# Kernel optimization log

Hardware: AMD Instinct MI355X
Metric: run time of the kernel (lower is better)

Reference implementation:

```python
import jax, jax.numpy as jnp
import numpy as np

B, N, M, T, D, NH = 64, 1024, 32, 8, 512, 8
OUT = 1000
NSO, NSA = N // 4, N // 8
DH = D // NH


def _conv(x, w, b):
    y = jax.lax.conv_general_dilated(x, w, (1, 1), 'SAME', dimension_numbers=('NCHW', 'OIHW', 'NCHW'))
    return y + b[None, :, None, None]


def _bn(x, g, b):
    # BatchNorm2d in train mode: per-batch statistics over (B, H, W)
    m = x.mean(axis=(0, 2, 3), keepdims=True)
    v = x.var(axis=(0, 2, 3), keepdims=True)
    return (x - m) * jax.lax.rsqrt(v + 1e-5) * g[None, :, None, None] + b[None, :, None, None]


def _mp2(x):
    b_, c, h, w = x.shape
    return x.reshape(b_, c, h // 2, 2, w // 2, 2).max(axis=(3, 5))


def _ln(x, g, b):
    m = x.mean(-1, keepdims=True)
    v = x.var(-1, keepdims=True)
    return (x - m) * jax.lax.rsqrt(v + 1e-5) * g + b


def _glu(x):
    a, b = jnp.split(x, 2, axis=-1)
    return a * jax.nn.sigmoid(b)


def setup_inputs():
    ks = iter(jax.random.split(jax.random.key(0), 64))

    def nrm(shape, fan_in):
        return jax.random.normal(next(ks), shape, jnp.float32) / np.float32(np.sqrt(fan_in))

    inp = {}
    inp['x'] = jax.random.normal(next(ks), (B, 3, 64, 64), jnp.float32)
    inp['c1w'] = nrm((16, 3, 3, 3), 27); inp['c1b'] = jnp.zeros((16,))
    inp['bn1g'] = jnp.ones((16,)); inp['bn1b'] = jnp.zeros((16,))
    inp['c2w'] = nrm((32, 16, 3, 3), 144); inp['c2b'] = jnp.zeros((32,))
    inp['bn2g'] = jnp.ones((32,)); inp['bn2b'] = jnp.zeros((32,))
    inp['c3w'] = nrm((64, 32, 3, 3), 288); inp['c3b'] = jnp.zeros((64,))
    inp['bn3g'] = jnp.ones((64,)); inp['bn3b'] = jnp.zeros((64,))
    inp['c4w'] = nrm((64, 64, 3, 3), 576); inp['c4b'] = jnp.zeros((64,))
    inp['bn4g'] = jnp.ones((64,)); inp['bn4b'] = jnp.zeros((64,))
    inp['fc1w'] = nrm((256, 256), 256); inp['fc1b'] = jnp.zeros((256,))
    inp['fc2w'] = nrm((128, D), 128); inp['fc2b'] = jnp.zeros((D,))
    inp['kvw'] = nrm((D, D), D); inp['kvb'] = jnp.zeros((D,))
    inp['kvlg'] = jnp.ones((D,)); inp['kvlb'] = jnp.zeros((D,))
    inp['synw'] = nrm((D + N, 2 * N), D + N); inp['synb'] = jnp.zeros((2 * N,))
    inp['synlg'] = jnp.ones((N,)); inp['synlb'] = jnp.zeros((N,))
    inp['nlm_w1'] = nrm((N, M, 256), M); inp['nlm_b1'] = jnp.zeros((N, 256))
    inp['nlm_w2'] = nrm((N, 128), 128); inp['nlm_b2'] = jnp.zeros((N,))
    inp['start_act'] = nrm((N,), N)
    inp['start_trace'] = nrm((N, M), N + M)
    inp['dec_a'] = jax.random.uniform(next(ks), (NSA,), jnp.float32, 0.0, 3.0)
    inp['dec_o'] = jax.random.uniform(next(ks), (NSO,), jnp.float32, 0.0, 3.0)
    inp['qw'] = nrm((NSA, D), NSA); inp['qb'] = jnp.zeros((D,))
    inp['attn_inw'] = nrm((D, 3 * D), D); inp['attn_inb'] = jnp.zeros((3 * D,))
    inp['attn_ow'] = nrm((D, D), D); inp['attn_ob'] = jnp.zeros((D,))
    inp['op_w1'] = nrm((NSO, 256), NSO); inp['op_b1'] = jnp.zeros((256,))
    inp['op_l1g'] = jnp.ones((256,)); inp['op_l1b'] = jnp.zeros((256,))
    inp['op_w2'] = nrm((256, 64), 256); inp['op_b2'] = jnp.zeros((64,))
    inp['op_l2g'] = jnp.ones((64,)); inp['op_l2b'] = jnp.zeros((64,))
    inp['op_w3'] = nrm((64, OUT), 64); inp['op_b3'] = jnp.zeros((OUT,))
    inp['aL'] = jax.random.randint(next(ks), (NSA,), 0, N)
    inp['aR'] = jax.random.randint(next(ks), (NSA,), 0, N)
    inp['oL'] = jax.random.randint(next(ks), (NSO,), 0, N)
    inp['oR'] = jax.random.randint(next(ks), (NSO,), 0, N)
    inp['task_idx'] = 0
    return inp


def _forward(x, c1w, c1b, bn1g, bn1b, c2w, c2b, bn2g, bn2b, c3w, c3b, bn3g, bn3b, c4w, c4b, bn4g, bn4b, fc1w, fc1b, fc2w, fc2b, kvw, kvb, kvlg, kvlb, synw, synb, synlg, synlb, nlm_w1, nlm_b1, nlm_w2, nlm_b2, start_act, start_trace, dec_a, dec_o, qw, qb, attn_inw, attn_inb, attn_ow, attn_ob, op_w1, op_b1, op_l1g, op_l1b, op_w2, op_b2, op_l2g, op_l2b, op_w3, op_b3, aL, aR, oL, oR):
    # --- AdaptiveCNNEncoder (3-channel branch) ---
    h = jax.nn.relu(_bn(_conv(x, c1w, c1b), bn1g, bn1b))
    h = jax.nn.relu(_bn(_conv(h, c2w, c2b), bn2g, bn2b))
    h = _mp2(h)
    h = jax.nn.relu(_bn(_conv(h, c3w, c3b), bn3g, bn3b))
    h = _mp2(h)
    h = jax.nn.relu(_bn(_conv(h, c4w, c4b), bn4g, bn4b))
    b_, c, hh, ww = h.shape
    # AdaptiveAvgPool2d((2,2)): mean over equal blocks (16x16 -> 2x2)
    h = h.reshape(b_, c, 2, hh // 2, 2, ww // 2).mean(axis=(3, 5)).reshape(b_, c * 4)
    enc = _glu(h @ fc1w + fc1b) @ fc2w + fc2b            # (B, D)
    kv = _ln(enc @ kvw + kvb, kvlg, kvlb)                # single kv token

    Wq, Wk, Wv = jnp.split(attn_inw, 3, axis=1)
    bq, bk, bv = jnp.split(attn_inb, 3)
    kh = (kv @ Wk + bk).reshape(B, NH, DH)
    vh = (kv @ Wv + bv).reshape(B, NH, DH)

    r_a = jnp.exp(-jnp.clip(dec_a, 0.0, 15.0))           # (NSA,)
    r_o = jnp.exp(-jnp.clip(dec_o, 0.0, 15.0))           # (NSO,)

    act0 = jnp.broadcast_to(start_act, (B, N))
    trace0 = jnp.broadcast_to(start_trace, (B, N, M))
    ao0 = act0[:, oL] * act0[:, oR]                      # initial out-sync accumulators
    bo0 = jnp.ones_like(ao0)
    inv_log_out = np.float32(1.0 / np.log(OUT))
    inv_sqrt_dh = np.float32(1.0 / np.sqrt(DH))

    def tick(carry, t):
        act, trace, aa, ba, ao, bo = carry
        pp = act[:, aL] * act[:, aR]
        first = (t == 0)
        aa = jnp.where(first, pp, r_a * aa + pp)
        ba = jnp.where(first, jnp.ones_like(ba), r_a * ba + 1.0)
        sync_a = aa * jax.lax.rsqrt(ba + 1e-8)
        qv = sync_a @ qw + qb
        qh = (qv @ Wq + bq).reshape(B, NH, DH)
        logits = jnp.einsum('bhd,bhd->bh', qh, kh) * inv_sqrt_dh
        w = jax.nn.softmax(logits[..., None], axis=-1)[..., 0]  # single key -> ones
        attn_out = (w[..., None] * vh).reshape(B, D) @ attn_ow + attn_ob
        pre = jnp.concatenate([attn_out, act], axis=-1)
        state = _ln(_glu(pre @ synw + synb), synlg, synlb)
        trace = jnp.concatenate([trace[:, :, 1:], state[:, :, None]], axis=-1)
        # per-neuron private MLPs, batched: (B,N,M)x(N,M,256) -> GLU -> (N,128) -> scalar
        hid = _glu(jnp.einsum('bnm,nmh->bnh', trace, nlm_w1) + nlm_b1)
        act = jnp.einsum('bnh,nh->bn', hid, nlm_w2) + nlm_b2
        po = act[:, oL] * act[:, oR]
        ao = r_o * ao + po
        bo = r_o * bo + 1.0
        sync_o = ao * jax.lax.rsqrt(bo + 1e-8)
        h1 = jax.nn.relu(_ln(sync_o @ op_w1 + op_b1, op_l1g, op_l1b))
        h2 = jax.nn.relu(_ln(h1 @ op_w2 + op_b2, op_l2g, op_l2b))
        pred = h2 @ op_w3 + op_b3
        p = jax.nn.softmax(pred, axis=-1)
        ent = -jnp.sum(p * jnp.log(p + 1e-10), axis=-1)
        ne = ent * inv_log_out
        cert = jnp.stack([ne, 1.0 - ne], axis=-1)
        return (act, trace, aa, ba, ao, bo), (pred, cert)

    carry0 = (act0, trace0, jnp.zeros((B, NSA), jnp.float32), jnp.zeros((B, NSA), jnp.float32), ao0, bo0)
    _, (preds, certs) = jax.lax.scan(tick, carry0, jnp.arange(T))
    return jnp.transpose(preds, (1, 2, 0)), jnp.transpose(certs, (1, 2, 0))


def reference(x, c1w, c1b, bn1g, bn1b, c2w, c2b, bn2g, bn2b, c3w, c3b, bn3g, bn3b, c4w, c4b, bn4g, bn4b, fc1w, fc1b, fc2w, fc2b, kvw, kvb, kvlg, kvlb, synw, synb, synlg, synlb, nlm_w1, nlm_b1, nlm_w2, nlm_b2, start_act, start_trace, dec_a, dec_o, qw, qb, attn_inw, attn_inb, attn_ow, attn_ob, op_w1, op_b1, op_l1g, op_l1b, op_w2, op_b2, op_l2g, op_l2b, op_w3, op_b3, aL, aR, oL, oR, task_idx):
    del task_idx  # single task; all task-indexed params are for task 0
    return _forward(x, c1w, c1b, bn1g, bn1b, c2w, c2b, bn2g, bn2b, c3w, c3b, bn3g, bn3b, c4w, c4b, bn4g, bn4b, fc1w, fc1b, fc2w, fc2b, kvw, kvb, kvlg, kvlb, synw, synb, synlg, synlb, nlm_w1, nlm_b1, nlm_w2, nlm_b2, start_act, start_trace, dec_a, dec_o, qw, qb, attn_inw, attn_inb, attn_ow, attn_ob, op_w1, op_b1, op_l1g, op_l1b, op_w2, op_b2, op_l2g, op_l2b, op_w3, op_b3, aL, aR, oL, oR)
```

## Files before the change

kernel.cpp:

```cpp
#include <hip/hip_runtime.h>
#include <math.h>

constexpr int B_ = 64, N_ = 1024, M_ = 32, T_ = 8;
constexpr int OUT_ = 1000, NSO_ = 256;

#define DEVFN __device__ __forceinline__

typedef __attribute__((ext_vector_type(8))) short bf16x8;
typedef __attribute__((ext_vector_type(4))) float f32x4;

DEVFN float blockReduceSum(float v, float* buf) {
  int t = threadIdx.x;
  buf[t] = v; __syncthreads();
  for (int off = blockDim.x >> 1; off > 0; off >>= 1) {
    if (t < off) buf[t] += buf[t + off];
    __syncthreads();
  }
  float r = buf[0];
  __syncthreads();
  return r;
}

DEVFN float sigmoidf_(float x) { return 1.f / (1.f + __expf(-x)); }

DEVFN unsigned short f2bf(float f) {
  unsigned u = __float_as_uint(f);
  unsigned r = (u + 0x7FFFu + ((u >> 16) & 1u)) >> 16;
  return (unsigned short)r;
}
DEVFN float bf2f(unsigned short h) { return __uint_as_float((unsigned)h << 16); }

template<int NW>
DEVFN float bsum(float v, float* red) {
  #pragma unroll
  for (int o = 32; o > 0; o >>= 1) v += __shfl_xor(v, o);
  int w = threadIdx.x >> 6, ln = threadIdx.x & 63;
  if (ln == 0) red[w] = v;
  __syncthreads();
  if (w == 0) {
    float x = (ln < NW) ? red[ln] : 0.f;
    #pragma unroll
    for (int o = 8; o > 0; o >>= 1) x += __shfl_xor(x, o);
    if (ln == 0) red[0] = x;
  }
  __syncthreads();
  float r = red[0];
  __syncthreads();
  return r;
}

template<int NW>
DEVFN float bmax(float v, float* red) {
  #pragma unroll
  for (int o = 32; o > 0; o >>= 1) v = fmaxf(v, __shfl_xor(v, o));
  int w = threadIdx.x >> 6, ln = threadIdx.x & 63;
  if (ln == 0) red[w] = v;
  __syncthreads();
  if (w == 0) {
    float x = (ln < NW) ? red[ln] : -INFINITY;
    #pragma unroll
    for (int o = 8; o > 0; o >>= 1) x = fmaxf(x, __shfl_xor(x, o));
    if (ln == 0) red[0] = x;
  }
  __syncthreads();
  float r = red[0];
  __syncthreads();
  return r;
}

DEVFN void bn_ssl(float2* ssl, const float* bnpart, const float* g, const float* bb,
                  int C, int ns, float inv_n) {
  for (int c = threadIdx.x; c < C; c += blockDim.x) {
    float s1 = 0.f, s2 = 0.f;
    for (int s = 0; s < ns; ++s) { s1 += bnpart[(c * ns + s) * 2]; s2 += bnpart[(c * ns + s) * 2 + 1]; }
    float m = s1 * inv_n;
    float var = s2 * inv_n - m * m;
    float rstd = rsqrtf(var + 1e-5f);
    float sc = g[c] * rstd;
    ssl[c] = make_float2(sc, bb[c] - m * sc);
  }
}

__global__ __launch_bounds__(256)
void k_wprep(const float* __restrict__ c2w, const float* __restrict__ c3w,
             const float* __restrict__ c4w, unsigned short* __restrict__ wt2,
             unsigned short* __restrict__ wt3, unsigned short* __restrict__ wt4) {
  int i = blockIdx.x * 256 + threadIdx.x;
  if (i < 5120) {
    int tap = i / 512, co = (i / 16) % 32, ci = i & 15;
    wt2[i] = (tap < 9) ? f2bf(c2w[(co * 16 + ci) * 9 + tap]) : 0;
  } else if (i < 5120 + 18432) {
    int j = i - 5120;
    int tap = j / 2048, co = (j / 32) % 64, ci = j & 31;
    wt3[j] = f2bf(c3w[(co * 32 + ci) * 9 + tap]);
  } else if (i < 5120 + 18432 + 36864) {
    int j = i - 5120 - 18432;
    int tap = j / 4096, co = (j / 64) % 64, ci = j & 63;
    wt4[j] = f2bf(c4w[(co * 64 + ci) * 9 + tap]);
  }
}

__global__ __launch_bounds__(256)
void k_w1t(const float* __restrict__ w1, unsigned short* __restrict__ w1t) {
  int n = blockIdx.x;
  __shared__ float tile[32][260];
  const float* src = w1 + (size_t)n * 8192;
  for (int i = threadIdx.x; i < 8192; i += 256)
    tile[i >> 8][i & 255] = src[i];
  __syncthreads();
  int c = threadIdx.x;
  unsigned short* dst = w1t + ((size_t)n * 256 + c) * 32;
  #pragma unroll
  for (int q = 0; q < 8; ++q) {
    ushort4 o;
    o.x = f2bf(tile[q * 4 + 0][c]); o.y = f2bf(tile[q * 4 + 1][c]);
    o.z = f2bf(tile[q * 4 + 2][c]); o.w = f2bf(tile[q * 4 + 3][c]);
    *reinterpret_cast<ushort4*>(dst + q * 4) = o;
  }
}

__global__ __launch_bounds__(256)
void k_synwt(const float* __restrict__ synw2, unsigned short* __restrict__ Bt) {
  int j0 = blockIdx.x * 64, k0 = blockIdx.y * 64;
  __shared__ float tile[64][65];
  for (int i = threadIdx.x; i < 4096; i += 256) {
    int kk = i >> 6, jj = i & 63;
    tile[kk][jj] = synw2[(size_t)(k0 + kk) * 2048 + j0 + jj];
  }
  __syncthreads();
  int jj = threadIdx.x >> 2, kq = (threadIdx.x & 3) * 16;
  unsigned short* dst = Bt + (size_t)(j0 + jj) * 1024 + k0 + kq;
  #pragma unroll
  for (int q = 0; q < 4; ++q) {
    ushort4 o;
    o.x = f2bf(tile[kq + q * 4 + 0][jj]); o.y = f2bf(tile[kq + q * 4 + 1][jj]);
    o.z = f2bf(tile[kq + q * 4 + 2][jj]); o.w = f2bf(tile[kq + q * 4 + 3][jj]);
    *reinterpret_cast<ushort4*>(dst + q * 4) = o;
  }
}

__global__ __launch_bounds__(256)
void k_conv1(const float* __restrict__ in, const float* __restrict__ wgl,
             unsigned short* __restrict__ outp) {
  constexpr int HW = 64, TY = 4, XV = 4, XQ = 16, CPT = 4;
  __shared__ __align__(16) float ins[3][TY + 2][HW + 8];
  const int b = blockIdx.x, y0 = blockIdx.y * TY, tid = threadIdx.x;
  const int sp = tid & 63;
  const int cg = __builtin_amdgcn_readfirstlane(tid >> 6);
  const int xq = sp % XQ, yr = sp / XQ, x0 = xq * XV;
  float acc[CPT][XV];
  #pragma unroll
  for (int j = 0; j < CPT; ++j)
    #pragma unroll
    for (int k = 0; k < XV; ++k) acc[j][k] = 0.f;
  constexpr int NEL = 3 * (TY + 2) * (HW + 8);
  for (int i = tid; i < NEL; i += 256) {
    int col = i % (HW + 8), row = (i / (HW + 8)) % (TY + 2), ci = i / ((HW + 8) * (TY + 2));
    int gx = col - 4, gy = y0 + row - 1;
    float v = 0.f;
    if (gx >= 0 && gx < HW && gy >= 0 && gy < HW)
      v = in[((size_t)(b * 3 + ci) * HW + gy) * HW + gx];
    ins[ci][row][col] = v;
  }
  __syncthreads();
  for (int ci = 0; ci < 3; ++ci) {
    const float* wci = wgl + ((size_t)(cg * CPT) * 3 + ci) * 9;
    #pragma unroll
    for (int dy = 0; dy < 3; ++dy) {
      const float* r = &ins[ci][yr + dy][x0 + 4];
      float win[6];
      win[0] = r[-1];
      float4 m = *reinterpret_cast<const float4*>(r);
      win[1] = m.x; win[2] = m.y; win[3] = m.z; win[4] = m.w;
      win[5] = r[4];
      #pragma unroll
      for (int j = 0; j < CPT; ++j) {
        const float* wj = wci + (size_t)j * 27 + dy * 3;
        float w0 = wj[0], w1 = wj[1], w2 = wj[2];
        #pragma unroll
        for (int k = 0; k < XV; ++k)
          acc[j][k] = fmaf(win[k], w0, fmaf(win[k + 1], w1, fmaf(win[k + 2], w2, acc[j][k])));
      }
    }
  }
  #pragma unroll
  for (int j = 0; j < CPT; ++j) {
    unsigned short* op = outp + (((size_t)b * 16 + cg * CPT + j) * HW + y0 + yr) * HW + x0;
    ushort4 o;
    o.x = f2bf(acc[j][0]); o.y = f2bf(acc[j][1]); o.z = f2bf(acc[j][2]); o.w = f2bf(acc[j][3]);
    *reinterpret_cast<ushort4*>(op) = o;
  }
}

__global__ __launch_bounds__(256)
void k_conv2_mfma(const unsigned short* __restrict__ in, const unsigned short* __restrict__ wt2,
                  const float* __restrict__ bnpart, const float* __restrict__ bng,
                  const float* __restrict__ bnb, unsigned short* __restrict__ outp) {
  const int b = blockIdx.x, y = blockIdx.y;
  const int tid = threadIdx.x;
  const int w = tid >> 6, lane = tid & 63;
  const int col = lane & 15, kg = lane >> 4;
  const int p0 = w * 16;
  __shared__ unsigned short lds[3][68][16];
  __shared__ float2 ssl[16];
  bn_ssl(ssl, bnpart, bng, bnb, 16, 32, 1.f / (float)(B_ * 4096));
  __syncthreads();
  for (int i = tid; i < 3 * 66 * 16; i += 256) {
    int px = i % 66, row = (i / 66) % 3, ci = i / 198;
    int gy = y + row - 1, gx = px - 1;
    float v = 0.f;
    if (gy >= 0 && gy < 64 && gx >= 0 && gx < 64) {
      float2 s = ssl[ci];
      v = fmaxf(fmaf(bf2f(in[((size_t)(b * 16 + ci) * 64 + gy) * 64 + gx]), s.x, s.y), 0.f);
    }
    lds[row][px][ci] = f2bf(v);
  }
  __syncthreads();
  f32x4 acc0 = {0.f, 0.f, 0.f, 0.f}, acc1 = {0.f, 0.f, 0.f, 0.f};
  const int tsel = kg >> 1, ci0 = (kg & 1) * 8;
  #pragma unroll
  for (int p = 0; p < 5; ++p) {
    int tap = 2 * p + tsel;
    int dy = (tap < 9) ? tap / 3 : 0;
    int dx = (tap < 9) ? tap % 3 : 0;
    bf16x8 af = *reinterpret_cast<const bf16x8*>(&lds[dy][p0 + col + dx][ci0]);
    bf16x8 b0 = *reinterpret_cast<const bf16x8*>(wt2 + ((size_t)tap * 32 + col) * 16 + ci0);
    bf16x8 b1 = *reinterpret_cast<const bf16x8*>(wt2 + ((size_t)tap * 32 + 16 + col) * 16 + ci0);
    acc0 = __builtin_amdgcn_mfma_f32_16x16x32_bf16(af, b0, acc0, 0, 0, 0);
    acc1 = __builtin_amdgcn_mfma_f32_16x16x32_bf16(af, b1, acc1, 0, 0, 0);
  }
  int px = p0 + kg * 4;
  ushort4 o0, o1;
  o0.x = f2bf(acc0[0]); o0.y = f2bf(acc0[1]); o0.z = f2bf(acc0[2]); o0.w = f2bf(acc0[3]);
  o1.x = f2bf(acc1[0]); o1.y = f2bf(acc1[1]); o1.z = f2bf(acc1[2]); o1.w = f2bf(acc1[3]);
  *reinterpret_cast<ushort4*>(outp + ((size_t)(b * 32 + col) * 64 + y) * 64 + px) = o0;
  *reinterpret_cast<ushort4*>(outp + ((size_t)(b * 32 + 16 + col) * 64 + y) * 64 + px) = o1;
}

__global__ __launch_bounds__(256)
void k_conv3_mfma(const unsigned short* __restrict__ in, const unsigned short* __restrict__ wt3,
                  const float* __restrict__ bnpart, const float* __restrict__ bng,
                  const float* __restrict__ bnb, unsigned short* __restrict__ outp) {
  const int b = blockIdx.x, y0 = blockIdx.y * 2;
  const int tid = threadIdx.x;
  const int w = tid >> 6, lane = tid & 63;
  const int col = lane & 15, kg = lane >> 4;
  const int yloc = w >> 1, p0 = (w & 1) * 16;
  __shared__ unsigned short lds[4][34][40];
  __shared__ float2 ssl[32];
  bn_ssl(ssl, bnpart, bng, bnb, 32, 32, 1.f / (float)(B_ * 4096));
  __syncthreads();
  for (int i = tid; i < 4 * 34 * 32; i += 256) {
    int px = i % 34, row = (i / 34) % 4, ci = i / 136;
    int gy = y0 + row - 1, gx = px - 1;
    float v = 0.f;
    if (gy >= 0 && gy < 32 && gx >= 0 && gx < 32) {
      float2 s = ssl[ci];
      size_t base = ((size_t)(b * 32 + ci) * 64 + 2 * gy) * 64 + 2 * gx;
      float r0 = fmaf(bf2f(in[base]),      s.x, s.y);
      float r1 = fmaf(bf2f(in[base + 1]),  s.x, s.y);
      float r2 = fmaf(bf2f(in[base + 64]), s.x, s.y);
      float r3 = fmaf(bf2f(in[base + 65]), s.x, s.y);
      v = fmaxf(fmaxf(fmaxf(r0, r1), fmaxf(r2, r3)), 0.f);
    }
    lds[row][px][ci] = f2bf(v);
  }
  __syncthreads();
  f32x4 acc[4];
  #pragma unroll
  for (int c = 0; c < 4; ++c) acc[c] = (f32x4){0.f, 0.f, 0.f, 0.f};
  #pragma unroll
  for (int tap = 0; tap < 9; ++tap) {
    int dy = tap / 3, dx = tap % 3;
    bf16x8 af = *reinterpret_cast<const bf16x8*>(&lds[yloc + dy][p0 + col + dx][kg * 8]);
    #pragma unroll
    for (int c = 0; c < 4; ++c) {
      bf16x8 bfr = *reinterpret_cast<const bf16x8*>(wt3 + ((size_t)tap * 64 + c * 16 + col) * 32 + kg * 8);
      acc[c] = __builtin_amdgcn_mfma_f32_16x16x32_bf16(af, bfr, acc[c], 0, 0, 0);
    }
  }
  int yy = y0 + yloc, px = p0 + kg * 4;
  #pragma unroll
  for (int c = 0; c < 4; ++c) {
    ushort4 o;
    o.x = f2bf(acc[c][0]); o.y = f2bf(acc[c][1]); o.z = f2bf(acc[c][2]); o.w = f2bf(acc[c][3]);
    *reinterpret_cast<ushort4*>(outp + ((size_t)(b * 64 + c * 16 + col) * 32 + yy) * 32 + px) = o;
  }
}

__global__ __launch_bounds__(128)
void k_conv4_mfma(const unsigned short* __restrict__ in, const unsigned short* __restrict__ wt4,
                  const float* __restrict__ bnpart, const float* __restrict__ bng,
                  const float* __restrict__ bnb, unsigned short* __restrict__ outp) {
  const int b = blockIdx.x, y0 = blockIdx.y * 2;
  const int tid = threadIdx.x;
  const int w = tid >> 6, lane = tid & 63;
  const int col = lane & 15, kg = lane >> 4;
  __shared__ unsigned short lds[4][18][72];
  __shared__ float2 ssl[64];
  bn_ssl(ssl, bnpart, bng, bnb, 64, 16, 1.f / (float)(B_ * 1024));
  __syncthreads();
  for (int i = tid; i < 4 * 18 * 64; i += 128) {
    int px = i % 18, row = (i / 18) % 4, ci = i / 72;
    int gy = y0 + row - 1, gx = px - 1;
    float v = 0.f;
    if (gy >= 0 && gy < 16 && gx >= 0 && gx < 16) {
      float2 s = ssl[ci];
      size_t base = ((size_t)(b * 64 + ci) * 32 + 2 * gy) * 32 + 2 * gx;
      float r0 = fmaf(bf2f(in[base]),      s.x, s.y);
      float r1 = fmaf(bf2f(in[base + 1]),  s.x, s.y);
      float r2 = fmaf(bf2f(in[base + 32]), s.x, s.y);
      float r3 = fmaf(bf2f(in[base + 33]), s.x, s.y);
      v = fmaxf(fmaxf(fmaxf(r0, r1), fmaxf(r2, r3)), 0.f);
    }
    lds[row][px][ci] = f2bf(v);
  }
  __syncthreads();
  f32x4 acc[4];
  #pragma unroll
  for (int c = 0; c < 4; ++c) acc[c] = (f32x4){0.f, 0.f, 0.f, 0.f};
  #pragma unroll
  for (int tap = 0; tap < 9; ++tap) {
    int dy = tap / 3, dx = tap % 3;
    #pragma unroll
    for (int kc = 0; kc < 2; ++kc) {
      bf16x8 af = *reinterpret_cast<const bf16x8*>(&lds[w + dy][col + dx][kc * 32 + kg * 8]);
      #pragma unroll
      for (int c = 0; c < 4; ++c) {
        bf16x8 bfr = *reinterpret_cast<const bf16x8*>(wt4 + ((size_t)tap * 64 + c * 16 + col) * 64 + kc * 32 + kg * 8);
        acc[c] = __builtin_amdgcn_mfma_f32_16x16x32_bf16(af, bfr, acc[c], 0, 0, 0);
      }
    }
  }
  int yy = y0 + w, px = kg * 4;
  #pragma unroll
  for (int c = 0; c < 4; ++c) {
    ushort4 o;
    o.x = f2bf(acc[c][0]); o.y = f2bf(acc[c][1]); o.z = f2bf(acc[c][2]); o.w = f2bf(acc[c][3]);
    *reinterpret_cast<ushort4*>(outp + ((size_t)(b * 64 + c * 16 + col) * 16 + yy) * 16 + px) = o;
  }
}

template<int C, int HW2>
__global__ __launch_bounds__(256)
void k_bn_stats_bf(const unsigned short* __restrict__ x, float* __restrict__ part) {
  int c = blockIdx.x, s = blockIdx.y, ns = gridDim.y;
  const int Np2 = B_ * HW2 / 2;
  float s1 = 0.f, s2 = 0.f;
  for (int ii = s * 256 + threadIdx.x; ii < Np2; ii += ns * 256) {
    int b = ii / (HW2 / 2), p2 = ii % (HW2 / 2);
    const unsigned short* pp = x + ((size_t)b * C + c) * HW2 + p2 * 2;
    unsigned u = *reinterpret_cast<const unsigned*>(pp);
    float v0 = __uint_as_float(u << 16);
    float v1 = __uint_as_float(u & 0xFFFF0000u);
    s1 += v0 + v1; s2 += v0 * v0 + v1 * v1;
  }
  __shared__ float r1[256], r2[256];
  r1[threadIdx.x] = s1; r2[threadIdx.x] = s2; __syncthreads();
  for (int off = 128; off > 0; off >>= 1) {
    if (threadIdx.x < off) { r1[threadIdx.x] += r1[threadIdx.x + off]; r2[threadIdx.x] += r2[threadIdx.x + off]; }
    __syncthreads();
  }
  if (threadIdx.x == 0) {
    part[(c * ns + s) * 2 + 0] = r1[0];
    part[(c * ns + s) * 2 + 1] = r2[0];
  }
}

__global__ __launch_bounds__(256)
void k_avgpool_bn_bf(const unsigned short* __restrict__ x, const float* __restrict__ bnpart,
                     const float* __restrict__ g, const float* __restrict__ bb,
                     float* __restrict__ outp) {
  __shared__ float2 ssl[64];
  bn_ssl(ssl, bnpart, g, bb, 64, 8, 1.f / (float)(B_ * 256));
  __syncthreads();
  int idx = blockIdx.x * 256 + threadIdx.x;
  int b = idx >> 8;
  int r = idx & 255;
  int c = r >> 2, i = (r >> 1) & 1, j = r & 1;
  float2 s = ssl[c];
  const unsigned short* p = x + ((size_t)(b * 64 + c) * 16 + i * 8) * 16 + j * 8;
  float sum = 0.f;
  #pragma unroll
  for (int yy = 0; yy < 8; ++yy)
    #pragma unroll
    for (int xx = 0; xx < 8; ++xx)
      sum += fmaxf(fmaf(bf2f(p[yy * 16 + xx]), s.x, s.y), 0.f);
  outp[idx] = sum * (1.f / 64.f);
}

template<int K, int NOUT>
__global__ __launch_bounds__(256)
void k_gemm_part(const float* __restrict__ A, const float* __restrict__ W, int ldw,
                 float* __restrict__ part) {
  int jt = blockIdx.x, ks = blockIdx.y;
  int k0 = ks * 64;
  __shared__ float As[64][65];
  for (int i = threadIdx.x; i < 4096; i += 256) {
    int r = i >> 6, c = i & 63;
    As[r][c] = A[(size_t)r * K + k0 + c];
  }
  __syncthreads();
  int jsub = threadIdx.x & 31;
  int bg = threadIdx.x >> 5;
  int j = jt * 32 + jsub;
  float acc[8] = {0.f, 0.f, 0.f, 0.f, 0.f, 0.f, 0.f, 0.f};
  const float* wp = W + (size_t)k0 * ldw + j;
  #pragma unroll 8
  for (int kk = 0; kk < 64; ++kk) {
    float w = wp[(size_t)kk * ldw];
    #pragma unroll
    for (int r = 0; r < 8; ++r) acc[r] = fmaf(As[bg * 8 + r][kk], w, acc[r]);
  }
  float* pp = part + (size_t)ks * 64 * NOUT + j;
  #pragma unroll
  for (int r = 0; r < 8; ++r) pp[(size_t)(bg * 8 + r) * NOUT] = acc[r];
}

__global__ __launch_bounds__(256)
void k_syn_mfma(const unsigned short* __restrict__ Abf, const unsigned short* __restrict__ Bt,
                float* __restrict__ part) {
  const int jt = blockIdx.x, ks = blockIdx.y;
  const int w = threadIdx.x >> 6, lane = threadIdx.x & 63;
  const int col = lane & 15, kg = lane >> 4;
  const int jcol = jt * 64 + w * 16 + col;
  const int k0 = ks * 256;
  f32x4 acc[4];
  #pragma unroll
  for (int mt = 0; mt < 4; ++mt) acc[mt] = (f32x4){0.f, 0.f, 0.f, 0.f};
  #pragma unroll
  for (int kb = 0; kb < 8; ++kb) {
    const int kk = k0 + kb * 32 + kg * 8;
    bf16x8 bfr = *reinterpret_cast<const bf16x8*>(Bt + (size_t)jcol * 1024 + kk);
    #pragma unroll
    for (int mt = 0; mt < 4; ++mt) {
      bf16x8 a = *reinterpret_cast<const bf16x8*>(Abf + (size_t)(mt * 16 + col) * 1024 + kk);
      acc[mt] = __builtin_amdgcn_mfma_f32_16x16x32_bf16(a, bfr, acc[mt], 0, 0, 0);
    }
  }
  #pragma unroll
  for (int mt = 0; mt < 4; ++mt) {
    int b0 = mt * 16 + kg * 4;
    #pragma unroll
    for (int r = 0; r < 4; ++r)
      part[((size_t)ks * 64 + b0 + r) * 2048 + jcol] = acc[mt][r];
  }
}

template<int NOUT, int NO_FIN, int KS, bool GLU_, bool LN_>
__global__ __launch_bounds__(256)
void k_fc_reduce(const float* __restrict__ part, const float* __restrict__ bias, int bstride,
                 const float* __restrict__ lng, const float* __restrict__ lnb,
                 float* __restrict__ outp) {
  constexpr int R = (NO_FIN + 255) / 256;
  int b = blockIdx.x, t = threadIdx.x;
  const float* bp = bias + (size_t)b * bstride;
  float v[R];
  #pragma unroll
  for (int r = 0; r < R; ++r) {
    int j = t + r * 256;
    if (j < NO_FIN) {
      float za = bp[j];
      float zb = GLU_ ? bp[j + NO_FIN] : 0.f;
      #pragma unroll
      for (int ks = 0; ks < KS; ++ks) {
        const float* pr = part + ((size_t)ks * 64 + b) * NOUT;
        za += pr[j];
        if (GLU_) zb += pr[j + NO_FIN];
      }
      v[r] = GLU_ ? za * sigmoidf_(zb) : za;
    } else v[r] = 0.f;
  }
  if (LN_) {
    __shared__ float red[256];
    float s1 = 0.f, s2 = 0.f;
    #pragma unroll
    for (int r = 0; r < R; ++r) { s1 += v[r]; s2 += v[r] * v[r]; }
    s1 = blockReduceSum(s1, red);
    s2 = blockReduceSum(s2, red);
    float mu = s1 / (float)NO_FIN;
    float rstd = rsqrtf(s2 / (float)NO_FIN - mu * mu + 1e-5f);
    #pragma unroll
    for (int r = 0; r < R; ++r) {
      int j = t + r * 256;
      if (j < NO_FIN) outp[(size_t)b * NO_FIN + j] = fmaf((v[r] - mu) * rstd, lng[j], lnb[j]);
    }
  } else {
    #pragma unroll
    for (int r = 0; r < R; ++r) {
      int j = t + r * 256;
      if (j < NO_FIN) outp[(size_t)b * NO_FIN + j] = v[r];
    }
  }
}

__global__ __launch_bounds__(1024)
void k_syn_reduce(const float* __restrict__ part, const float* __restrict__ syncst,
                  const float* __restrict__ g, const float* __restrict__ bb,
                  unsigned short* __restrict__ trace, int slot) {
  int b = blockIdx.x, t = threadIdx.x;
  __shared__ float red[16];
  float za = syncst[b * 2048 + t];
  float zb = syncst[b * 2048 + 1024 + t];
  #pragma unroll
  for (int ks = 0; ks < 4; ++ks) {
    const float* pr = part + ((size_t)ks * 64 + b) * 2048;
    za += pr[t];
    zb += pr[t + 1024];
  }
  float v = za * sigmoidf_(zb);
  float s1 = bsum<16>(v, red);
  float s2 = bsum<16>(v * v, red);
  float mu = s1 * (1.f / 1024.f);
  float rstd = rsqrtf(s2 * (1.f / 1024.f) - mu * mu + 1e-5f);
  trace[((size_t)t * 64 + b) * 32 + slot] = f2bf(fmaf((v - mu) * rstd, g[t], bb[t]));
}

__global__ __launch_bounds__(256)
void k_init(const float* __restrict__ sa, const float* __restrict__ st,
            const int* __restrict__ oL, const int* __restrict__ oR,
            float* __restrict__ act, unsigned short* __restrict__ act_bf,
            unsigned short* __restrict__ trace,
            float* __restrict__ ao, float* __restrict__ bo) {
  int idx = blockIdx.x * 256 + threadIdx.x;
  if (idx < B_ * N_ * M_) {
    int n = idx >> 11, m = idx & 31;
    trace[idx] = f2bf(st[n * 32 + m]);
  }
  if (idx < B_ * N_) {
    float v = sa[idx % N_];
    act[idx] = v;
    act_bf[idx] = f2bf(v);
  }
  if (idx < B_ * NSO_) {
    int i = idx % NSO_;
    ao[idx] = sa[oL[i]] * sa[oR[i]];
    bo[idx] = 1.f;
  }
}

__global__ __launch_bounds__(128)
void k_nlm_mfma(const unsigned short* __restrict__ trace, const unsigned short* __restrict__ w1t,
                const float* __restrict__ b1, const float* __restrict__ w2,
                const float* __restrict__ b2, float* __restrict__ act,
                unsigned short* __restrict__ act_bf, int tick) {
  const int w = threadIdx.x >> 6, lane = threadIdx.x & 63;
  const int n = blockIdx.x * 2 + w;
  const int col = lane & 15, kg = lane >> 4;
  __shared__ __align__(16) unsigned short ldsA[2][64][40];
  {
    const uint4* src = reinterpret_cast<const uint4*>(trace + ((size_t)n * 64 + lane) * 32);
    uint4 r0 = src[0], r1 = src[1], r2 = src[2], r3 = src[3];
    uint4* d = reinterpret_cast<uint4*>(&ldsA[w][lane][0]);
    d[0] = r0; d[1] = r1; d[2] = r2; d[3] = r3;
  }
  bf16x8 bf[16];
  float b1v[16], w2v[8];
  #pragma unroll
  for (int nt = 0; nt < 16; ++nt) {
    bf[nt] = *reinterpret_cast<const bf16x8*>(w1t + (((size_t)n * 256 + nt * 16 + col) * 32 + kg * 8));
    b1v[nt] = b1[n * 256 + nt * 16 + col];
  }
  #pragma unroll
  for (int nt = 0; nt < 8; ++nt) w2v[nt] = w2[n * 128 + nt * 16 + col];
  const float b2n = b2[n];
  const int kbase = kg * 8 + ((tick + 1) & 31);
  __syncthreads();
  #pragma unroll
  for (int mt = 0; mt < 4; ++mt) {
    const int brow = mt * 16 + col;
    bf16x8 af;
    #pragma unroll
    for (int j = 0; j < 8; ++j)
      af[j] = (short)ldsA[w][brow][(kbase + j) & 31];
    f32x4 acc[16];
    #pragma unroll
    for (int nt = 0; nt < 16; ++nt)
      acc[nt] = __builtin_amdgcn_mfma_f32_16x16x32_bf16(af, bf[nt], (f32x4){0.f, 0.f, 0.f, 0.f}, 0, 0, 0);
    float v0 = 0.f, v1 = 0.f, v2 = 0.f, v3 = 0.f;
    #pragma unroll
    for (int nt = 0; nt < 8; ++nt) {
      f32x4 za = acc[nt], zb = acc[nt + 8];
      float ba = b1v[nt], bg = b1v[nt + 8], wv = w2v[nt];
      v0 = fmaf((za[0] + ba) * sigmoidf_(zb[0] + bg), wv, v0);
      v1 = fmaf((za[1] + ba) * sigmoidf_(zb[1] + bg), wv, v1);
      v2 = fmaf((za[2] + ba) * sigmoidf_(zb[2] + bg), wv, v2);
      v3 = fmaf((za[3] + ba) * sigmoidf_(zb[3] + bg), wv, v3);
    }
    #pragma unroll
    for (int o = 1; o <= 8; o <<= 1) {
      v0 += __shfl_xor(v0, o); v1 += __shfl_xor(v1, o);
      v2 += __shfl_xor(v2, o); v3 += __shfl_xor(v3, o);
    }
    if (col == 0) {
      int b0 = mt * 16 + kg * 4;
      float r0 = v0 + b2n, r1 = v1 + b2n, r2 = v2 + b2n, r3 = v3 + b2n;
      act[(size_t)(b0 + 0) * 1024 + n] = r0;
      act[(size_t)(b0 + 1) * 1024 + n] = r1;
      act[(size_t)(b0 + 2) * 1024 + n] = r2;
      act[(size_t)(b0 + 3) * 1024 + n] = r3;
      act_bf[(size_t)(b0 + 0) * 1024 + n] = f2bf(r0);
      act_bf[(size_t)(b0 + 1) * 1024 + n] = f2bf(r1);
      act_bf[(size_t)(b0 + 2) * 1024 + n] = f2bf(r2);
      act_bf[(size_t)(b0 + 3) * 1024 + n] = f2bf(r3);
    }
  }
}

__global__ __launch_bounds__(1024)
void k_outpath(const float* __restrict__ act, float* __restrict__ ao, float* __restrict__ bo,
               const float* __restrict__ dec_o, const int* __restrict__ oL, const int* __restrict__ oR,
               const float* __restrict__ opw1, const float* __restrict__ opb1,
               const float* __restrict__ l1g, const float* __restrict__ l1b,
               const float* __restrict__ opw2, const float* __restrict__ opb2,
               const float* __restrict__ l2g, const float* __restrict__ l2b,
               const float* __restrict__ opw3, const float* __restrict__ opb3,
               float* __restrict__ outp, int tick) {
  int b = blockIdx.x, t = threadIdx.x;
  __shared__ float red[16];
  __shared__ float syo[256], h1s[256], h2s[64];
  __shared__ float zp1[4][256];
  __shared__ float zp2[16][64];
  const float* actb = act + (size_t)b * 1024;
  if (t < 256) {
    float po = actb[oL[t]] * actb[oR[t]];
    float r = __expf(-fminf(fmaxf(dec_o[t], 0.f), 15.f));
    int ai = b * 256 + t;
    float av = fmaf(r, ao[ai], po);
    float bv = fmaf(r, bo[ai], 1.f);
    ao[ai] = av; bo[ai] = bv;
    syo[t] = av * rsqrtf(bv + 1e-8f);
  }
  __syncthreads();
  {
    int j = t & 255, ks = t >> 8;
    float z = 0.f;
    const float* wcol = opw1 + j;
    #pragma unroll 8
    for (int k = ks * 64; k < ks * 64 + 64; ++k) z = fmaf(syo[k], wcol[k * 256], z);
    zp1[ks][j] = z;
  }
  __syncthreads();
  float h1v = 0.f;
  if (t < 256) h1v = zp1[0][t] + zp1[1][t] + zp1[2][t] + zp1[3][t] + opb1[t];
  float s1 = bsum<16>(t < 256 ? h1v : 0.f, red);
  float s2 = bsum<16>(t < 256 ? h1v * h1v : 0.f, red);
  if (t < 256) {
    float mu = s1 * (1.f / 256.f);
    float rstd = rsqrtf(s2 * (1.f / 256.f) - mu * mu + 1e-5f);
    h1s[t] = fmaxf(fmaf((h1v - mu) * rstd, l1g[t], l1b[t]), 0.f);
  }
  __syncthreads();
  {
    int j = t & 63, ks = t >> 6;
    float z = 0.f;
    const float* wcol = opw2 + j;
    #pragma unroll
    for (int k = ks * 16; k < ks * 16 + 16; ++k) z = fmaf(h1s[k], wcol[k * 64], z);
    zp2[ks][j] = z;
  }
  __syncthreads();
  if (t < 64) {
    float z2 = opb2[t];
    #pragma unroll
    for (int ks = 0; ks < 16; ++ks) z2 += zp2[ks][t];
    float a1 = z2, a2 = z2 * z2;
    #pragma unroll
    for (int o = 32; o > 0; o >>= 1) { a1 += __shfl_xor(a1, o); a2 += __shfl_xor(a2, o); }
    float mu2 = a1 * (1.f / 64.f);
    float rs2 = rsqrtf(a2 * (1.f / 64.f) - mu2 * mu2 + 1e-5f);
    h2s[t] = fmaxf(fmaf((z2 - mu2) * rs2, l2g[t], l2b[t]), 0.f);
  }
  __syncthreads();
  float z3 = 0.f;
  if (t < OUT_) {
    z3 = opb3[t];
    const float* wcol = opw3 + t;
    #pragma unroll 8
    for (int k = 0; k < 64; ++k) z3 = fmaf(h2s[k], wcol[k * OUT_], z3);
    outp[(size_t)b * (OUT_ * T_) + (size_t)t * T_ + tick] = z3;
  }
  float mx = bmax<16>(t < OUT_ ? z3 : -INFINITY, red);
  float e = (t < OUT_) ? __expf(z3 - mx) : 0.f;
  float S = bsum<16>(e, red);
  float inv = 1.f / S;
  float ep = 0.f;
  if (t < OUT_) {
    float p = e * inv;
    ep = p * __logf(p + 1e-10f);
  }
  float ent = -bsum<16>(ep, red);
  if (t == 0) {
    float ne = ent * (1.f / logf(1000.f));
    outp[(size_t)B_ * OUT_ * T_ + (size_t)b * 2 * T_ + tick]      = ne;
    outp[(size_t)B_ * OUT_ * T_ + (size_t)b * 2 * T_ + T_ + tick] = 1.f - ne;
  }
}

extern "C" void kernel_launch(void* const* d_in, const int* in_sizes, int n_in,
                              void* d_out, int out_size, void* d_ws, size_t ws_size,
                              hipStream_t stream) {
  (void)in_sizes; (void)n_in; (void)out_size; (void)ws_size;
  const float* x      = (const float*)d_in[0];
  const float* c1w    = (const float*)d_in[1];
  const float* bn1g   = (const float*)d_in[3];
  const float* bn1b   = (const float*)d_in[4];
  const float* c2w    = (const float*)d_in[5];
  const float* bn2g   = (const float*)d_in[7];
  const float* bn2b   = (const float*)d_in[8];
  const float* c3w    = (const float*)d_in[9];
  const float* bn3g   = (const float*)d_in[11];
  const float* bn3b   = (const float*)d_in[12];
  const float* c4w    = (const float*)d_in[13];
  const float* bn4g   = (const float*)d_in[15];
  const float* bn4b   = (const float*)d_in[16];
  const float* fc1w   = (const float*)d_in[17];
  const float* fc1b   = (const float*)d_in[18];
  const float* fc2w   = (const float*)d_in[19];
  const float* fc2b   = (const float*)d_in[20];
  const float* kvw    = (const float*)d_in[21];
  const float* kvb    = (const float*)d_in[22];
  const float* kvlg   = (const float*)d_in[23];
  const float* kvlb   = (const float*)d_in[24];
  const float* synw   = (const float*)d_in[25];
  const float* synb   = (const float*)d_in[26];
  const float* synlg  = (const float*)d_in[27];
  const float* synlb  = (const float*)d_in[28];
  const float* nlmw1  = (const float*)d_in[29];
  const float* nlmb1  = (const float*)d_in[30];
  const float* nlmw2  = (const float*)d_in[31];
  const float* nlmb2  = (const float*)d_in[32];
  const float* sact   = (const float*)d_in[33];
  const float* strc   = (const float*)d_in[34];
  const float* dec_o  = (const float*)d_in[36];
  const float* attn_inw = (const float*)d_in[39];
  const float* attn_inb = (const float*)d_in[40];
  const float* attn_ow  = (const float*)d_in[41];
  const float* attn_ob  = (const float*)d_in[42];
  const float* opw1   = (const float*)d_in[43];
  const float* opb1   = (const float*)d_in[44];
  const float* opl1g  = (const float*)d_in[45];
  const float* opl1b  = (const float*)d_in[46];
  const float* opw2   = (const float*)d_in[47];
  const float* opb2   = (const float*)d_in[48];
  const float* opl2g  = (const float*)d_in[49];
  const float* opl2b  = (const float*)d_in[50];
  const float* opw3   = (const float*)d_in[51];
  const float* opb3   = (const float*)d_in[52];
  const int*   oL     = (const int*)d_in[55];
  const int*   oR     = (const int*)d_in[56];
  float* outp = (float*)d_out;
  float* ws   = (float*)d_ws;

  unsigned short* c1raw_bf = (unsigned short*)(ws + 8388608);
  unsigned short* c2raw_bf = (unsigned short*)ws;
  unsigned short* c3raw_bf = (unsigned short*)(ws + 8388608);
  unsigned short* c4raw_bf = (unsigned short*)ws;
  float* part  = ws + 4194304;
  unsigned short* trace_bf = (unsigned short*)(ws + 6291456);
  float* act   = ws + 8388608;
  float* syncst= ws + 8454144;
  float* pooled= ws + 8585216;
  float* ench  = ws + 8601600;
  float* enc   = ws + 8609792;
  float* kvbuf = ws + 8642560;
  float* vhbuf = ws + 8675328;
  float* aout  = ws + 8708096;
  float* ao    = ws + 8740864;
  float* bo    = ws + 8757248;
  unsigned short* w1t_bf   = (unsigned short*)(ws + 8777728);
  unsigned short* synw2t_bf= (unsigned short*)(ws + 12972032);
  unsigned short* wt2 = (unsigned short*)(ws + 14061568);
  unsigned short* wt3 = (unsigned short*)(ws + 14064128);
  unsigned short* wt4 = (unsigned short*)(ws + 14073344);
  float* bnpart = ws + 14091776;
  unsigned short* act_bf = (unsigned short*)(ws + 14095872);

  k_wprep<<<236,256,0,stream>>>(c2w, c3w, c4w, wt2, wt3, wt4);

  k_conv1<<<dim3(64,16),256,0,stream>>>(x, c1w, c1raw_bf);
  k_bn_stats_bf<16,4096><<<dim3(16,32),256,0,stream>>>(c1raw_bf, bnpart);

  k_conv2_mfma<<<dim3(64,64),256,0,stream>>>(c1raw_bf, wt2, bnpart, bn1g, bn1b, c2raw_bf);
  k_bn_stats_bf<32,4096><<<dim3(32,32),256,0,stream>>>(c2raw_bf, bnpart);

  k_conv3_mfma<<<dim3(64,16),256,0,stream>>>(c2raw_bf, wt3, bnpart, bn2g, bn2b, c3raw_bf);
  k_bn_stats_bf<64,1024><<<dim3(64,16),256,0,stream>>>(c3raw_bf, bnpart);

  k_conv4_mfma<<<dim3(64,8),128,0,stream>>>(c3raw_bf, wt4, bnpart, bn3g, bn3b, c4raw_bf);

  k_w1t<<<1024,256,0,stream>>>(nlmw1, w1t_bf);
  k_synwt<<<dim3(32,16),256,0,stream>>>(synw + (size_t)512 * 2048, synw2t_bf);

  k_bn_stats_bf<64,256><<<dim3(64,8),256,0,stream>>>(c4raw_bf, bnpart);
  k_avgpool_bn_bf<<<64,256,0,stream>>>(c4raw_bf, bnpart, bn4g, bn4b, pooled);

  k_gemm_part<256,256><<<dim3(8,4),256,0,stream>>>(pooled, fc1w, 256, part);
  k_fc_reduce<256,128,4,true,false><<<64,256,0,stream>>>(part, fc1b, 0, nullptr, nullptr, ench);
  k_gemm_part<128,512><<<dim3(16,2),256,0,stream>>>(ench, fc2w, 512, part);
  k_fc_reduce<512,512,2,false,false><<<64,256,0,stream>>>(part, fc2b, 0, nullptr, nullptr, enc);
  k_gemm_part<512,512><<<dim3(16,8),256,0,stream>>>(enc, kvw, 512, part);
  k_fc_reduce<512,512,8,false,true><<<64,256,0,stream>>>(part, kvb, 0, kvlg, kvlb, kvbuf);
  k_gemm_part<512,512><<<dim3(16,8),256,0,stream>>>(kvbuf, attn_inw + 1024, 1536, part);
  k_fc_reduce<512,512,8,false,false><<<64,256,0,stream>>>(part, attn_inb + 1024, 0, nullptr, nullptr, vhbuf);
  k_gemm_part<512,512><<<dim3(16,8),256,0,stream>>>(vhbuf, attn_ow, 512, part);
  k_fc_reduce<512,512,8,false,false><<<64,256,0,stream>>>(part, attn_ob, 0, nullptr, nullptr, aout);
  k_gemm_part<512,2048><<<dim3(64,8),256,0,stream>>>(aout, synw, 2048, part);
  k_fc_reduce<2048,2048,8,false,false><<<64,256,0,stream>>>(part, synb, 0, nullptr, nullptr, syncst);

  k_init<<<8192,256,0,stream>>>(sact, strc, oL, oR, act, act_bf, trace_bf, ao, bo);

  for (int t = 0; t < T_; ++t) {
    k_syn_mfma<<<dim3(32,4),256,0,stream>>>(act_bf, synw2t_bf, part);
    k_syn_reduce<<<64,1024,0,stream>>>(part, syncst, synlg, synlb, trace_bf, t);
    k_nlm_mfma<<<512,128,0,stream>>>(trace_bf, w1t_bf, nlmb1, nlmw2, nlmb2, act, act_bf, t);
    k_outpath<<<64,1024,0,stream>>>(act, ao, bo, dec_o, oL, oR,
                                    opw1, opb1, opl1g, opl1b,
                                    opw2, opb2, opl2g, opl2b,
                                    opw3, opb3, outp, t);
  }
}
```

Before: 527.0 us.

## Fuse encoder FC chain into single per-batch kernel

```diff
diff --git a/kernel.cpp b/kernel.cpp
--- a/kernel.cpp
+++ b/kernel.cpp
@@ -8,18 +8,6 @@
 
 typedef __attribute__((ext_vector_type(8))) short bf16x8;
 typedef __attribute__((ext_vector_type(4))) float f32x4;
-
-DEVFN float blockReduceSum(float v, float* buf) {
-  int t = threadIdx.x;
-  buf[t] = v; __syncthreads();
-  for (int off = blockDim.x >> 1; off > 0; off >>= 1) {
-    if (t < off) buf[t] += buf[t + off];
-    __syncthreads();
-  }
-  float r = buf[0];
-  __syncthreads();
-  return r;
-}
 
 DEVFN float sigmoidf_(float x) { return 1.f / (1.f + __expf(-x)); }
 
@@ -389,32 +377,99 @@
   outp[idx] = sum * (1.f / 64.f);
 }
 
-template<int K, int NOUT>
-__global__ __launch_bounds__(256)
-void k_gemm_part(const float* __restrict__ A, const float* __restrict__ W, int ldw,
-                 float* __restrict__ part) {
-  int jt = blockIdx.x, ks = blockIdx.y;
-  int k0 = ks * 64;
-  __shared__ float As[64][65];
-  for (int i = threadIdx.x; i < 4096; i += 256) {
-    int r = i >> 6, c = i & 63;
-    As[r][c] = A[(size_t)r * K + k0 + c];
-  }
-  __syncthreads();
-  int jsub = threadIdx.x & 31;
-  int bg = threadIdx.x >> 5;
-  int j = jt * 32 + jsub;
-  float acc[8] = {0.f, 0.f, 0.f, 0.f, 0.f, 0.f, 0.f, 0.f};
-  const float* wp = W + (size_t)k0 * ldw + j;
-  #pragma unroll 8
-  for (int kk = 0; kk < 64; ++kk) {
-    float w = wp[(size_t)kk * ldw];
-    #pragma unroll
-    for (int r = 0; r < 8; ++r) acc[r] = fmaf(As[bg * 8 + r][kk], w, acc[r]);
-  }
-  float* pp = part + (size_t)ks * 64 * NOUT + j;
-  #pragma unroll
-  for (int r = 0; r < 8; ++r) pp[(size_t)(bg * 8 + r) * NOUT] = acc[r];
+__global__ __launch_bounds__(1024)
+void k_encfc(const float* __restrict__ pooled,
+             const float* __restrict__ fc1w, const float* __restrict__ fc1b,
+             const float* __restrict__ fc2w, const float* __restrict__ fc2b,
+             const float* __restrict__ kvw, const float* __restrict__ kvb,
+             const float* __restrict__ kvlg, const float* __restrict__ kvlb,
+             const float* __restrict__ attn_inw, const float* __restrict__ attn_inb,
+             const float* __restrict__ attn_ow, const float* __restrict__ attn_ob,
+             const float* __restrict__ synw, const float* __restrict__ synb,
+             float* __restrict__ syncst) {
+  const int b = blockIdx.x, t = threadIdx.x;
+  __shared__ float a[256], ench[128], enc[512], kv[512], vh[512], ao_[512];
+  __shared__ float zp[1024];
+  __shared__ float red[16];
+  if (t < 256) a[t] = pooled[b * 256 + t];
+  __syncthreads();
+  {
+    int j = t & 255, ks = t >> 8;
+    float z = 0.f;
+    const float* w = fc1w + j;
+    #pragma unroll 8
+    for (int k = ks * 64; k < ks * 64 + 64; ++k) z = fmaf(a[k], w[k * 256], z);
+    zp[ks * 256 + j] = z;
+  }
+  __syncthreads();
+  if (t < 128) {
+    float za = zp[t] + zp[256 + t] + zp[512 + t] + zp[768 + t] + fc1b[t];
+    int j2 = t + 128;
+    float zb = zp[j2] + zp[256 + j2] + zp[512 + j2] + zp[768 + j2] + fc1b[j2];
+    ench[t] = za * sigmoidf_(zb);
+  }
+  __syncthreads();
+  {
+    int j = t & 511, ks = t >> 9;
+    float z = 0.f;
+    const float* w = fc2w + j;
+    #pragma unroll 8
+    for (int k = ks * 64; k < ks * 64 + 64; ++k) z = fmaf(ench[k], w[k * 512], z);
+    zp[ks * 512 + j] = z;
+  }
+  __syncthreads();
+  if (t < 512) enc[t] = zp[t] + zp[512 + t] + fc2b[t];
+  __syncthreads();
+  {
+    int j = t & 511, ks = t >> 9;
+    float z = 0.f;
+    const float* w = kvw + j;
+    #pragma unroll 8
+    for (int k = ks * 256; k < ks * 256 + 256; ++k) z = fmaf(enc[k], w[k * 512], z);
+    zp[ks * 512 + j] = z;
+  }
+  __syncthreads();
+  float zkv = 0.f;
+  if (t < 512) zkv = zp[t] + zp[512 + t] + kvb[t];
+  float s1 = bsum<16>(t < 512 ? zkv : 0.f, red);
+  float s2 = bsum<16>(t < 512 ? zkv * zkv : 0.f, red);
+  if (t < 512) {
+    float mu = s1 * (1.f / 512.f);
+    float rstd = rsqrtf(s2 * (1.f / 512.f) - mu * mu + 1e-5f);
+    kv[t] = fmaf((zkv - mu) * rstd, kvlg[t], kvlb[t]);
+  }
+  __syncthreads();
+  {
+    int j = t & 511, ks = t >> 9;
+    float z = 0.f;
+    const float* w = attn_inw + 1024 + j;
+    #pragma unroll 8
+    for (int k = ks * 256; k < ks * 256 + 256; ++k) z = fmaf(kv[k], w[(size_t)k * 1536], z);
+    zp[ks * 512 + j] = z;
+  }
+  __syncthreads();
+  if (t < 512) vh[t] = zp[t] + zp[512 + t] + attn_inb[1024 + t];
+  __syncthreads();
+  {
+    int j = t & 511, ks = t >> 9;
+    float z = 0.f;
+    const float* w = attn_ow + j;
+    #pragma unroll 8
+    for (int k = ks * 256; k < ks * 256 + 256; ++k) z = fmaf(vh[k], w[k * 512], z);
+    zp[ks * 512 + j] = z;
+  }
+  __syncthreads();
+  if (t < 512) ao_[t] = zp[t] + zp[512 + t] + attn_ob[t];
+  __syncthreads();
+  #pragma unroll
+  for (int q = 0; q < 2; ++q) {
+    int j = t + q * 1024;
+    float z = synb[j];
+    const float* w = synw + j;
+    #pragma unroll 8
+    for (int k = 0; k < 512; ++k) z = fmaf(ao_[k], w[(size_t)k * 2048], z);
+    syncst[(size_t)b * 2048 + j] = z;
+  }
 }
 
 __global__ __launch_bounds__(256)
@@ -444,53 +499,6 @@
     #pragma unroll
     for (int r = 0; r < 4; ++r)
       part[((size_t)ks * 64 + b0 + r) * 2048 + jcol] = acc[mt][r];
-  }
-}
-
-template<int NOUT, int NO_FIN, int KS, bool GLU_, bool LN_>
-__global__ __launch_bounds__(256)
-void k_fc_reduce(const float* __restrict__ part, const float* __restrict__ bias, int bstride,
-                 const float* __restrict__ lng, const float* __restrict__ lnb,
-                 float* __restrict__ outp) {
-  constexpr int R = (NO_FIN + 255) / 256;
-  int b = blockIdx.x, t = threadIdx.x;
-  const float* bp = bias + (size_t)b * bstride;
-  float v[R];
-  #pragma unroll
-  for (int r = 0; r < R; ++r) {
-    int j = t + r * 256;
-    if (j < NO_FIN) {
-      float za = bp[j];
-      float zb = GLU_ ? bp[j + NO_FIN] : 0.f;
-      #pragma unroll
-      for (int ks = 0; ks < KS; ++ks) {
-        const float* pr = part + ((size_t)ks * 64 + b) * NOUT;
-        za += pr[j];
-        if (GLU_) zb += pr[j + NO_FIN];
-      }
-      v[r] = GLU_ ? za * sigmoidf_(zb) : za;
-    } else v[r] = 0.f;
-  }
-  if (LN_) {
-    __shared__ float red[256];
-    float s1 = 0.f, s2 = 0.f;
-    #pragma unroll
-    for (int r = 0; r < R; ++r) { s1 += v[r]; s2 += v[r] * v[r]; }
-    s1 = blockReduceSum(s1, red);
-    s2 = blockReduceSum(s2, red);
-    float mu = s1 / (float)NO_FIN;
-    float rstd = rsqrtf(s2 / (float)NO_FIN - mu * mu + 1e-5f);
-    #pragma unroll
-    for (int r = 0; r < R; ++r) {
-      int j = t + r * 256;
-      if (j < NO_FIN) outp[(size_t)b * NO_FIN + j] = fmaf((v[r] - mu) * rstd, lng[j], lnb[j]);
-    }
-  } else {
-    #pragma unroll
-    for (int r = 0; r < R; ++r) {
-      int j = t + r * 256;
-      if (j < NO_FIN) outp[(size_t)b * NO_FIN + j] = v[r];
-    }
   }
 }
 
@@ -761,11 +769,6 @@
   float* act   = ws + 8388608;
   float* syncst= ws + 8454144;
   float* pooled= ws + 8585216;
-  float* ench  = ws + 8601600;
-  float* enc   = ws + 8609792;
-  float* kvbuf = ws + 8642560;
-  float* vhbuf = ws + 8675328;
-  float* aout  = ws + 8708096;
   float* ao    = ws + 8740864;
   float* bo    = ws + 8757248;
   unsigned short* w1t_bf   = (unsigned short*)(ws + 8777728);
@@ -795,18 +798,10 @@
   k_bn_stats_bf<64,256><<<dim3(64,8),256,0,stream>>>(c4raw_bf, bnpart);
   k_avgpool_bn_bf<<<64,256,0,stream>>>(c4raw_bf, bnpart, bn4g, bn4b, pooled);
 
-  k_gemm_part<256,256><<<dim3(8,4),256,0,stream>>>(pooled, fc1w, 256, part);
-  k_fc_reduce<256,128,4,true,false><<<64,256,0,stream>>>(part, fc1b, 0, nullptr, nullptr, ench);
-  k_gemm_part<128,512><<<dim3(16,2),256,0,stream>>>(ench, fc2w, 512, part);
-  k_fc_reduce<512,512,2,false,false><<<64,256,0,stream>>>(part, fc2b, 0, nullptr, nullptr, enc);
-  k_gemm_part<512,512><<<dim3(16,8),256,0,stream>>>(enc, kvw, 512, part);
-  k_fc_reduce<512,512,8,false,true><<<64,256,0,stream>>>(part, kvb, 0, kvlg, kvlb, kvbuf);
-  k_gemm_part<512,512><<<dim3(16,8),256,0,stream>>>(kvbuf, attn_inw + 1024, 1536, part);
-  k_fc_reduce<512,512,8,false,false><<<64,256,0,stream>>>(part, attn_inb + 1024, 0, nullptr, nullptr, vhbuf);
-  k_gemm_part<512,512><<<dim3(16,8),256,0,stream>>>(vhbuf, attn_ow, 512, part);
-  k_fc_reduce<512,512,8,false,false><<<64,256,0,stream>>>(part, attn_ob, 0, nullptr, nullptr, aout);
-  k_gemm_part<512,2048><<<dim3(64,8),256,0,stream>>>(aout, synw, 2048, part);
-  k_fc_reduce<2048,2048,8,false,false><<<64,256,0,stream>>>(part, synb, 0, nullptr, nullptr, syncst);
+  k_encfc<<<64,1024,0,stream>>>(pooled, fc1w, fc1b, fc2w, fc2b,
+                                kvw, kvb, kvlg, kvlb,
+                                attn_inw, attn_inb, attn_ow, attn_ob,
+                                synw, synb, syncst);
 
   k_init<<<8192,256,0,stream>>>(sact, strc, oL, oR, act, act_bf, trace_bf, ao, bo);
 
```

Measured after the change: 559.4 us. 6.2% more time.
